# Kernel tuning notes

Measured on AMD Instinct MI355X. Metric: run time of the kernel, lower is better.

Reference implementation:

```python
import jax, jax.numpy as jnp
import numpy as np

D = 128
N_JOB, N_ST, N_MC, N_RB = 100000, 10000, 10000, 5000
E = 500000
RELS = [("cbl", N_ST), ("li", N_ST), ("nd", N_MC), ("eb", N_MC), ("hb", N_RB)]


def setup_inputs() -> dict:
    key = jax.random.key(0)
    ks = iter(jax.random.split(key, 64))
    inp = {
        "x_job": jax.random.normal(next(ks), (N_JOB, D), jnp.float32),
        "x_station": jax.random.normal(next(ks), (N_ST, D), jnp.float32),
        "x_machine": jax.random.normal(next(ks), (N_MC, D), jnp.float32),
        "x_robot": jax.random.normal(next(ks), (N_RB, D), jnp.float32),
    }
    for name, n_dst in RELS:
        inp[f"src_{name}"] = jax.random.randint(next(ks), (E,), 0, N_JOB, jnp.int32)
        inp[f"dst_{name}"] = jax.random.randint(next(ks), (E,), 0, n_dst, jnp.int32)
        # SAGEConv params: lin_l (with bias) on aggregated neighbors, lin_r (no bias) on dst
        inp[f"Wl_{name}"] = jax.random.normal(next(ks), (D, D), jnp.float32) * 0.02
        inp[f"bl_{name}"] = jnp.zeros((D,), jnp.float32)
        inp[f"Wr_{name}"] = jax.random.normal(next(ks), (D, D), jnp.float32) * 0.02
    return inp


def _sage(x_src, x_dst, src, dst, Wl, bl, Wr):
    # mean-aggregate source features over incoming edges, then linear + root linear
    n_dst = x_dst.shape[0]
    msg = x_src[src]                                                  # [E, D] gather
    agg = jax.ops.segment_sum(msg, dst, num_segments=n_dst)          # [n_dst, D]
    cnt = jax.ops.segment_sum(jnp.ones((src.shape[0],), x_src.dtype), dst, num_segments=n_dst)
    mean = agg / jnp.maximum(cnt, 1.0)[:, None]                       # isolated nodes -> 0
    return mean @ Wl.T + bl + x_dst @ Wr.T


def reference(x_job, x_station, x_machine, x_robot,
              src_cbl, dst_cbl, Wl_cbl, bl_cbl, Wr_cbl,
              src_li, dst_li, Wl_li, bl_li, Wr_li,
              src_nd, dst_nd, Wl_nd, bl_nd, Wr_nd,
              src_eb, dst_eb, Wl_eb, bl_eb, Wr_eb,
              src_hb, dst_hb, Wl_hb, bl_hb, Wr_hb):
    # HeteroConv aggr='sum' over relations sharing a destination type, then ReLU
    h_s = jax.nn.relu(_sage(x_job, x_station, src_cbl, dst_cbl, Wl_cbl, bl_cbl, Wr_cbl)
                      + _sage(x_job, x_station, src_li, dst_li, Wl_li, bl_li, Wr_li))
    h_m = jax.nn.relu(_sage(x_job, x_machine, src_nd, dst_nd, Wl_nd, bl_nd, Wr_nd)
                      + _sage(x_job, x_machine, src_eb, dst_eb, Wl_eb, bl_eb, Wr_eb))
    h_r = jax.nn.relu(_sage(x_job, x_robot, src_hb, dst_hb, Wl_hb, bl_hb, Wr_hb))
    return (h_s, h_m, h_r)
```

## Files before the change

kernel.cpp:

```cpp
#include <hip/hip_runtime.h>
#include <hip/hip_fp8.h>

#define D 128
#define NREL 5
#define E_EDGES 500000
#define NB_PER 313
#define NBTOT 1565
#define ST_CHUNK 8192
#define CAP 2048

typedef float f32x2 __attribute__((ext_vector_type(2)));
typedef __attribute__((ext_vector_type(8))) short bf16x8;
typedef __attribute__((ext_vector_type(4))) float f32x4;

struct RelIdx {
    const int* src[NREL];
    const int* dst[NREL];
};
struct MeanPtrs { float* mean[NREL]; };

__device__ __forceinline__ int shift_of(int r) { return (r < 4) ? 5 : 4; }

__device__ __forceinline__ unsigned char f32_to_fp8(float f) {
    __hip_fp8_e4m3 h(f);
    return (unsigned char)h.__x;
}
__device__ __forceinline__ float fp8_to_f32(unsigned int b) {
    __hip_fp8_e4m3 h;
    h.__x = (__hip_fp8_storage_t)b;
    return (float)h;
}
__device__ __forceinline__ unsigned short f2bf(float f) {
    unsigned u = __float_as_uint(f);
    unsigned r = (u + 0x7FFFu + ((u >> 16) & 1u)) >> 16;
    return (unsigned short)r;
}
#if defined(__has_builtin)
#if __has_builtin(__builtin_amdgcn_cvt_pk_f32_fp8)
#define HAVE_PK_CVT 1
#endif
#endif
template<bool HI>
__device__ __forceinline__ f32x2 pk8(unsigned u) {
#ifdef HAVE_PK_CVT
    return __builtin_amdgcn_cvt_pk_f32_fp8(u, HI);
#else
    unsigned s = HI ? (u >> 16) : u;
    f32x2 r; r.x = fp8_to_f32(s & 0xFF); r.y = fp8_to_f32((s >> 8) & 0xFF);
    return r;
#endif
}

struct PrepArgs {
    const float* Wl[NREL]; const float* Wr[NREL]; const float* bl[NREL];
    unsigned short* Bt0; unsigned short* Bt1; unsigned short* Bt2;
    float* bias;
};

struct FusedAArgs {
    RelIdx ri;
    int* bucket_cnt;
    const float* x_job; unsigned char* x_f8; int do_cvt;
    PrepArgs P;
    int nb_hist, nb_cvt;
};

__global__ __launch_bounds__(256) void fusedA_kernel(FusedAArgs A) {
    const int b = blockIdx.x;
    const int tid = threadIdx.x;
    if (b < A.nb_hist) {
        __shared__ int lh[NBTOT];
        for (int i = tid; i < NBTOT; i += 256) lh[i] = 0;
        __syncthreads();
        int e0 = (b * 256 + tid) * 4;
        if (e0 < E_EDGES) {
            #pragma unroll
            for (int r = 0; r < NREL; ++r) {
                int4 d4 = *reinterpret_cast<const int4*>(A.ri.dst[r] + e0);
                int sh = shift_of(r);
                atomicAdd(&lh[NB_PER * r + (d4.x >> sh)], 1);
                atomicAdd(&lh[NB_PER * r + (d4.y >> sh)], 1);
                atomicAdd(&lh[NB_PER * r + (d4.z >> sh)], 1);
                atomicAdd(&lh[NB_PER * r + (d4.w >> sh)], 1);
            }
        }
        __syncthreads();
        for (int i = tid; i < NBTOT; i += 256)
            if (lh[i]) atomicAdd(&A.bucket_cnt[i], lh[i]);
    } else if (b < A.nb_hist + A.nb_cvt) {
        if (!A.do_cvt) return;
        int t = (b - A.nb_hist) * 256 + tid;
        const int n8 = 100000 * D / 8;
        if (t >= n8) return;
        const float4* x4 = reinterpret_cast<const float4*>(A.x_job);
        float4 va = x4[2 * t], vb = x4[2 * t + 1];
        uint2 o;
        o.x = (unsigned)f32_to_fp8(va.x) | ((unsigned)f32_to_fp8(va.y) << 8)
            | ((unsigned)f32_to_fp8(va.z) << 16) | ((unsigned)f32_to_fp8(va.w) << 24);
        o.y = (unsigned)f32_to_fp8(vb.x) | ((unsigned)f32_to_fp8(vb.y) << 8)
            | ((unsigned)f32_to_fp8(vb.z) << 16) | ((unsigned)f32_to_fp8(vb.w) << 24);
        reinterpret_cast<uint2*>(A.x_f8)[t] = o;
    } else {
        int idx = (b - A.nb_hist - A.nb_cvt) * 256 + tid;
        const PrepArgs& P = A.P;
        if (idx < 49152) {
            int j = idx / 384, k = idx - j * 384;
            float v;
            if (k < 128)      v = P.Wl[0][j * D + k];
            else if (k < 256) v = P.Wl[1][j * D + (k - 128)];
            else              v = P.Wr[0][j * D + (k - 256)] + P.Wr[1][j * D + (k - 256)];
            P.Bt0[idx] = f2bf(v);
        } else if (idx < 98304) {
            int l = idx - 49152;
            int j = l / 384, k = l - j * 384;
            float v;
            if (k < 128)      v = P.Wl[2][j * D + k];
            else if (k < 256) v = P.Wl[3][j * D + (k - 128)];
            else              v = P.Wr[2][j * D + (k - 256)] + P.Wr[3][j * D + (k - 256)];
            P.Bt1[l] = f2bf(v);
        } else if (idx < 131072) {
            int l = idx - 98304;
            int j = l >> 8, k = l & 255;
            float v = (k < 128) ? P.Wl[4][j * D + k] : P.Wr[4][j * D + (k - 128)];
            P.Bt2[l] = f2bf(v);
        } else if (idx < 131456) {
            int l = idx - 131072;
            int t2 = l >> 7, j = l & 127;
            float v = (t2 == 0) ? P.bl[0][j] + P.bl[1][j]
                    : (t2 == 1) ? P.bl[2][j] + P.bl[3][j]
                                : P.bl[4][j];
            P.bias[l] = v;
        }
    }
}

__global__ __launch_bounds__(1024) void bucket_scan_kernel(
    const int* __restrict__ bucket_cnt, int* __restrict__ bucket_base,
    int* __restrict__ cur_b)
{
    __shared__ int s[1024];
    const int tid = threadIdx.x;
    const int i0 = 2 * tid, i1 = 2 * tid + 1;
    int c0 = (i0 < NBTOT) ? bucket_cnt[i0] : 0;
    int c1 = (i1 < NBTOT) ? bucket_cnt[i1] : 0;
    s[tid] = c0 + c1;
    __syncthreads();
    for (int d = 1; d < 1024; d <<= 1) {
        int t = (tid >= d) ? s[tid - d] : 0;
        __syncthreads();
        s[tid] += t;
        __syncthreads();
    }
    int exp_ = s[tid] - (c0 + c1);
    if (i0 < NBTOT) { bucket_base[i0] = exp_;      cur_b[i0] = exp_; }
    if (i1 < NBTOT) { bucket_base[i1] = exp_ + c0; cur_b[i1] = exp_ + c0; }
    if (tid == 1023) bucket_base[NBTOT] = s[1023];
}

__global__ __launch_bounds__(512) void stage_block_kernel(
    RelIdx idx, int* __restrict__ cur_b, int* __restrict__ stage)
{
    __shared__ int hist[NB_PER], gbase[NB_PER], lcur[NB_PER];
    const int tid = threadIdx.x;
    const int nchunk = (E_EDGES + ST_CHUNK - 1) / ST_CHUNK;
    const int r = blockIdx.x / nchunk;
    const int c = blockIdx.x - r * nchunk;
    const int e_beg = c * ST_CHUNK;
    const int e_end = min(e_beg + ST_CHUNK, E_EDGES);
    const int sh = shift_of(r);
    const int lmask = (1 << sh) - 1;
    for (int i = tid; i < NB_PER; i += 512) { hist[i] = 0; lcur[i] = 0; }
    __syncthreads();
    const int* dp = idx.dst[r];
    const int* sp = idx.src[r];

    int4 dreg[4];
    #pragma unroll
    for (int it = 0; it < 4; ++it) {
        int e = e_beg + tid * 4 + it * 2048;
        if (e + 4 <= e_end) {
            int4 d4 = *reinterpret_cast<const int4*>(dp + e);
            dreg[it] = d4;
            atomicAdd(&hist[d4.x >> sh], 1);
            atomicAdd(&hist[d4.y >> sh], 1);
            atomicAdd(&hist[d4.z >> sh], 1);
            atomicAdd(&hist[d4.w >> sh], 1);
        } else {
            for (int q = e; q < e_end; ++q) atomicAdd(&hist[dp[q] >> sh], 1);
        }
    }
    __syncthreads();

    for (int i = tid; i < NB_PER; i += 512)
        if (hist[i] > 0) gbase[i] = atomicAdd(&cur_b[NB_PER * r + i], hist[i]);
    __syncthreads();

    #pragma unroll
    for (int it = 0; it < 4; ++it) {
        int e = e_beg + tid * 4 + it * 2048;
        if (e + 4 <= e_end) {
            int4 d4 = dreg[it];
            int4 s4 = *reinterpret_cast<const int4*>(sp + e);
            int b0 = d4.x >> sh, p0 = gbase[b0] + atomicAdd(&lcur[b0], 1);
            stage[p0] = ((d4.x & lmask) << 20) | s4.x;
            int b1 = d4.y >> sh, p1 = gbase[b1] + atomicAdd(&lcur[b1], 1);
            stage[p1] = ((d4.y & lmask) << 20) | s4.y;
            int b2 = d4.z >> sh, p2 = gbase[b2] + atomicAdd(&lcur[b2], 1);
            stage[p2] = ((d4.z & lmask) << 20) | s4.z;
            int b3 = d4.w >> sh, p3 = gbase[b3] + atomicAdd(&lcur[b3], 1);
            stage[p3] = ((d4.w & lmask) << 20) | s4.w;
        } else {
            for (int q = e; q < e_end; ++q) {
                int dq = dp[q];
                int bq = dq >> sh, pq = gbase[bq] + atomicAdd(&lcur[bq], 1);
                stage[pq] = ((dq & lmask) << 20) | sp[q];
            }
        }
    }
}

template<bool FP8>
__global__ __launch_bounds__(256) void gather_bucket_kernel(
    const int* __restrict__ stage, const int* __restrict__ bucket_base,
    const void* __restrict__ xsrc, MeanPtrs mp)
{
    __shared__ int srt[CAP];
    __shared__ int h[32], ex[33], cur[32];
    const int b = blockIdx.x;
    const int tid = threadIdx.x;
    const int r = b / NB_PER;
    const int lb = b - NB_PER * r;
    const int sh = shift_of(r);
    const int ndst_r = (r < 4) ? 10000 : 5000;
    const int dst0 = lb << sh;
    const int nreal = min(1 << sh, ndst_r - dst0);
    const int seg0 = bucket_base[b];
    const int len = bucket_base[b + 1] - seg0;

    if (tid < 32) { h[tid] = 0; cur[tid] = 0; }
    __syncthreads();
    for (int p = tid; p < len; p += 256)
        atomicAdd(&h[stage[seg0 + p] >> 20], 1);
    __syncthreads();
    int c0 = (tid < 32) ? h[tid] : 0;
    for (int d = 1; d < 32; d <<= 1) {
        int t = (tid < 32 && tid >= d) ? h[tid - d] : 0;
        __syncthreads();
        if (tid < 32) h[tid] += t;
        __syncthreads();
    }
    if (tid < 32) ex[tid] = h[tid] - c0;
    if (tid == 0) ex[32] = len;
    __syncthreads();
    if (len <= CAP) {
        for (int p = tid; p < len; p += 256) {
            int v = stage[seg0 + p];
            int dl = v >> 20;
            int k = atomicAdd(&cur[dl], 1);
            srt[ex[dl] + k] = v & 0xFFFFF;
        }
    }
    __syncthreads();

    const int wave = tid >> 6, lane = tid & 63;
    float* mout = mp.mean[r];

    if (FP8) {
        const int quarter = lane >> 4, sub = lane & 15;
        const unsigned char* x8 = (const unsigned char*)xsrc;
        const unsigned char* xbase = x8 + sub * 8;
        for (int dl = wave; dl < nreal; dl += 4) {
            int s = ex[dl], e2 = ex[dl + 1];
            float4 aA = {0.f, 0.f, 0.f, 0.f};
            float4 aB = {0.f, 0.f, 0.f, 0.f};
            if (len <= CAP) {
                int k = s;
                for (; k + 8 <= e2; k += 8) {
                    int i0 = srt[k + quarter];
                    int i1 = srt[k + 4 + quarter];
                    uint2 u0 = *reinterpret_cast<const uint2*>(xbase + (size_t)i0 * D);
                    uint2 u1 = *reinterpret_cast<const uint2*>(xbase + (size_t)i1 * D);
                    f32x2 p0 = pk8<false>(u0.x), p1 = pk8<true>(u0.x);
                    f32x2 p2 = pk8<false>(u0.y), p3 = pk8<true>(u0.y);
                    f32x2 q0 = pk8<false>(u1.x), q1 = pk8<true>(u1.x);
                    f32x2 q2 = pk8<false>(u1.y), q3 = pk8<true>(u1.y);
                    aA.x += p0.x + q0.x; aA.y += p0.y + q0.y;
                    aA.z += p1.x + q1.x; aA.w += p1.y + q1.y;
                    aB.x += p2.x + q2.x; aB.y += p2.y + q2.y;
                    aB.z += p3.x + q3.x; aB.w += p3.y + q3.y;
                }
                for (; k < e2; k += 4) {
                    if (k + quarter < e2) {
                        int i0 = srt[k + quarter];
                        uint2 u = *reinterpret_cast<const uint2*>(xbase + (size_t)i0 * D);
                        f32x2 p0 = pk8<false>(u.x), p1 = pk8<true>(u.x);
                        f32x2 p2 = pk8<false>(u.y), p3 = pk8<true>(u.y);
                        aA.x += p0.x; aA.y += p0.y; aA.z += p1.x; aA.w += p1.y;
                        aB.x += p2.x; aB.y += p2.y; aB.z += p3.x; aB.w += p3.y;
                    }
                }
            } else {
                if (quarter == 0) {
                    for (int p = 0; p < len; ++p) {
                        int v = stage[seg0 + p];
                        if ((v >> 20) == dl) {
                            uint2 u = *reinterpret_cast<const uint2*>(
                                xbase + (size_t)(v & 0xFFFFF) * D);
                            f32x2 p0 = pk8<false>(u.x), p1 = pk8<true>(u.x);
                            f32x2 p2 = pk8<false>(u.y), p3 = pk8<true>(u.y);
                            aA.x += p0.x; aA.y += p0.y; aA.z += p1.x; aA.w += p1.y;
                            aB.x += p2.x; aB.y += p2.y; aB.z += p3.x; aB.w += p3.y;
                        }
                    }
                }
            }
            aA.x += __shfl_xor(aA.x, 16); aA.y += __shfl_xor(aA.y, 16);
            aA.z += __shfl_xor(aA.z, 16); aA.w += __shfl_xor(aA.w, 16);
            aB.x += __shfl_xor(aB.x, 16); aB.y += __shfl_xor(aB.y, 16);
            aB.z += __shfl_xor(aB.z, 16); aB.w += __shfl_xor(aB.w, 16);
            aA.x += __shfl_xor(aA.x, 32); aA.y += __shfl_xor(aA.y, 32);
            aA.z += __shfl_xor(aA.z, 32); aA.w += __shfl_xor(aA.w, 32);
            aB.x += __shfl_xor(aB.x, 32); aB.y += __shfl_xor(aB.y, 32);
            aB.z += __shfl_xor(aB.z, 32); aB.w += __shfl_xor(aB.w, 32);
            if (quarter == 0) {
                float inv = 1.0f / (float)max(e2 - s, 1);
                float4 m0, m1;
                m0.x = aA.x * inv; m0.y = aA.y * inv; m0.z = aA.z * inv; m0.w = aA.w * inv;
                m1.x = aB.x * inv; m1.y = aB.y * inv; m1.z = aB.z * inv; m1.w = aB.w * inv;
                float* orow = mout + (size_t)(dst0 + dl) * D + sub * 8;
                *reinterpret_cast<float4*>(orow) = m0;
                *reinterpret_cast<float4*>(orow + 4) = m1;
            }
        }
    } else {
        const float* basef = (const float*)xsrc + lane * 2;
        for (int dl = wave; dl < nreal; dl += 4) {
            int s = ex[dl], e2 = ex[dl + 1];
            float ax = 0.f, ay = 0.f;
            if (len <= CAP) {
                for (int k = s; k < e2; ++k) {
                    float2 v = *reinterpret_cast<const float2*>(basef + (size_t)srt[k] * D);
                    ax += v.x; ay += v.y;
                }
            } else {
                for (int p = 0; p < len; ++p) {
                    int v = stage[seg0 + p];
                    if ((v >> 20) == dl) {
                        float2 vv = *reinterpret_cast<const float2*>(basef + (size_t)(v & 0xFFFFF) * D);
                        ax += vv.x; ay += vv.y;
                    }
                }
            }
            float inv = 1.0f / (float)max(e2 - s, 1);
            float2 m; m.x = ax * inv; m.y = ay * inv;
            *reinterpret_cast<float2*>(mout + (size_t)(dst0 + dl) * D + lane * 2) = m;
        }
    }
}

struct GemmArgs {
    const float* Asrc[3][3];
    const unsigned short* Bt[3];
    const float* bias[3];
    float* out[3];
    int M[3]; int K[3]; int blk_start[3];
};

__global__ __launch_bounds__(256) void sage_gemm_kernel(GemmArgs A) {
    __shared__ unsigned short sA[64][40];
    __shared__ unsigned short sB[128][40];

    int b = blockIdx.x;
    int ty_ = (b >= A.blk_start[1]) + (b >= A.blk_start[2]);
    int mb = b - A.blk_start[ty_];
    const int M = A.M[ty_];
    const int K = A.K[ty_];
    const int row0 = mb * 64;
    const unsigned short* Bt = A.Bt[ty_];

    const int tid = threadIdx.x;
    const int lane = tid & 63;
    const int wave = tid >> 6;

    f32x4 acc[8];
    #pragma unroll
    for (int t = 0; t < 8; ++t) acc[t] = (f32x4){0.f, 0.f, 0.f, 0.f};

    for (int kc = 0; kc < K; kc += 32) {
        if (kc) __syncthreads();
        const float* src = A.Asrc[ty_][kc >> 7];
        const int c0 = kc & 127;

        {
            int r = tid >> 2, kg = (tid & 3) * 8;
            int grow = row0 + r; if (grow >= M) grow = M - 1;
            const float* p = src + (size_t)grow * D + c0 + kg;
            float4 v0 = *reinterpret_cast<const float4*>(p);
            float4 v1 = *reinterpret_cast<const float4*>(p + 4);
            uint4 w;
            w.x = (unsigned)f2bf(v0.x) | ((unsigned)f2bf(v0.y) << 16);
            w.y = (unsigned)f2bf(v0.z) | ((unsigned)f2bf(v0.w) << 16);
            w.z = (unsigned)f2bf(v1.x) | ((unsigned)f2bf(v1.y) << 16);
            w.w = (unsigned)f2bf(v1.z) | ((unsigned)f2bf(v1.w) << 16);
            *reinterpret_cast<uint4*>(&sA[r][kg]) = w;
        }
        #pragma unroll
        for (int i = 0; i < 2; ++i) {
            int s = tid + i * 256;
            int r = s >> 2, kg = (s & 3) * 8;
            *reinterpret_cast<uint4*>(&sB[r][kg]) =
                *reinterpret_cast<const uint4*>(Bt + (size_t)r * K + kc + kg);
        }
        __syncthreads();

        bf16x8 af = *reinterpret_cast<const bf16x8*>(&sA[wave * 16 + (lane & 15)][(lane >> 4) * 8]);
        #pragma unroll
        for (int t = 0; t < 8; ++t) {
            bf16x8 bfr = *reinterpret_cast<const bf16x8*>(&sB[t * 16 + (lane & 15)][(lane >> 4) * 8]);
            acc[t] = __builtin_amdgcn_mfma_f32_16x16x32_bf16(af, bfr, acc[t], 0, 0, 0);
        }
    }

    const float* bias = A.bias[ty_];
    float* out = A.out[ty_];
    const int c = lane & 15;
    const int rbase = wave * 16 + (lane >> 4) * 4;
    #pragma unroll
    for (int t = 0; t < 8; ++t) {
        int col = t * 16 + c;
        float bv = bias[col];
        #pragma unroll
        for (int q = 0; q < 4; ++q) {
            int grow = row0 + rbase + q;
            if (grow < M)
                out[(size_t)grow * D + col] = fmaxf(acc[t][q] + bv, 0.f);
        }
    }
}

extern "C" void kernel_launch(void* const* d_in, const int* in_sizes, int n_in,
                              void* d_out, int out_size, void* d_ws, size_t ws_size,
                              hipStream_t stream) {
    const float* x_job = (const float*)d_in[0];
    const float* x_st  = (const float*)d_in[1];
    const float* x_mc  = (const float*)d_in[2];
    const float* x_rb  = (const float*)d_in[3];

    const int N_JOB = 100000, N_ST = 10000, N_MC = 10000, N_RB = 5000;
    const int E = E_EDGES;

    RelIdx ri;
    const float* Wl[NREL]; const float* bl[NREL]; const float* Wr[NREL];
    for (int r = 0; r < NREL; ++r) {
        ri.src[r] = (const int*)  d_in[4 + r * 5 + 0];
        ri.dst[r] = (const int*)  d_in[4 + r * 5 + 1];
        Wl[r]     = (const float*)d_in[4 + r * 5 + 2];
        bl[r]     = (const float*)d_in[4 + r * 5 + 3];
        Wr[r]     = (const float*)d_in[4 + r * 5 + 4];
    }

    int* wsi = (int*)d_ws;
    float* wsf = (float*)d_ws;
    size_t off = 0;
    int* bucket_cnt  = wsi + off; off += NBTOT;
    int* bucket_base = wsi + off; off += NBTOT + 1;
    int* cur_b       = wsi + off; off += NBTOT;
    int* stage       = wsi + off; off += (size_t)NREL * E;
    float* mean_st_b = wsf + off; off += (size_t)N_ST * D;
    float* mean_mc_b = wsf + off; off += (size_t)N_MC * D;
    unsigned short* Bt0 = (unsigned short*)(wsi + off); off += 49152 / 2;
    unsigned short* Bt1 = (unsigned short*)(wsi + off); off += 49152 / 2;
    unsigned short* Bt2 = (unsigned short*)(wsi + off); off += 32768 / 2;
    float* bsum = wsf + off; off += 3 * 128;
    unsigned char* x_f8 = (unsigned char*)(wsi + off);
    size_t off_f8_end = off + (size_t)N_JOB * D / 4;
    const bool use_fp8 = (off_f8_end * sizeof(int) <= ws_size);

    float* out = (float*)d_out;
    MeanPtrs mp;
    mp.mean[0] = out;
    mp.mean[1] = mean_st_b;
    mp.mean[2] = out + (size_t)N_ST * D;
    mp.mean[3] = mean_mc_b;
    mp.mean[4] = out + (size_t)(N_ST + N_MC) * D;

    (void)hipMemsetAsync(bucket_cnt, 0, NBTOT * sizeof(int), stream);

    FusedAArgs FA;
    FA.ri = ri;
    FA.bucket_cnt = bucket_cnt;
    FA.x_job = x_job; FA.x_f8 = x_f8; FA.do_cvt = use_fp8 ? 1 : 0;
    for (int r = 0; r < NREL; ++r) { FA.P.Wl[r] = Wl[r]; FA.P.Wr[r] = Wr[r]; FA.P.bl[r] = bl[r]; }
    FA.P.Bt0 = Bt0; FA.P.Bt1 = Bt1; FA.P.Bt2 = Bt2; FA.P.bias = bsum;
    FA.nb_hist = (E / 4 + 255) / 256;
    FA.nb_cvt  = (N_JOB * D / 8 + 255) / 256;
    int nb_prep = (131456 + 255) / 256;
    fusedA_kernel<<<FA.nb_hist + FA.nb_cvt + nb_prep, 256, 0, stream>>>(FA);

    bucket_scan_kernel<<<1, 1024, 0, stream>>>(bucket_cnt, bucket_base, cur_b);

    const int nchunk = (E + ST_CHUNK - 1) / ST_CHUNK;
    stage_block_kernel<<<NREL * nchunk, 512, 0, stream>>>(ri, cur_b, stage);

    if (use_fp8)
        gather_bucket_kernel<true><<<NBTOT, 256, 0, stream>>>(stage, bucket_base, x_f8, mp);
    else
        gather_bucket_kernel<false><<<NBTOT, 256, 0, stream>>>(stage, bucket_base, x_job, mp);

    GemmArgs GA;
    GA.Asrc[0][0] = mp.mean[0]; GA.Asrc[0][1] = mp.mean[1]; GA.Asrc[0][2] = x_st;
    GA.Asrc[1][0] = mp.mean[2]; GA.Asrc[1][1] = mp.mean[3]; GA.Asrc[1][2] = x_mc;
    GA.Asrc[2][0] = mp.mean[4]; GA.Asrc[2][1] = x_rb;       GA.Asrc[2][2] = x_rb;
    GA.Bt[0] = Bt0; GA.Bt[1] = Bt1; GA.Bt[2] = Bt2;
    GA.bias[0] = bsum; GA.bias[1] = bsum + 128; GA.bias[2] = bsum + 256;
    GA.out[0] = out;
    GA.out[1] = out + (size_t)N_ST * D;
    GA.out[2] = out + (size_t)(N_ST + N_MC) * D;
    GA.M[0] = N_ST; GA.M[1] = N_MC; GA.M[2] = N_RB;
    GA.K[0] = 384;  GA.K[1] = 384;  GA.K[2] = 256;
    int nb0 = (N_ST + 63) / 64, nb1 = (N_MC + 63) / 64, nb2 = (N_RB + 63) / 64;
    GA.blk_start[0] = 0;
    GA.blk_start[1] = nb0;
    GA.blk_start[2] = nb0 + nb1;

    sage_gemm_kernel<<<nb0 + nb1 + nb2, 256, 0, stream>>>(GA);
}
```

Measured before the change: 146.2 us.

## Split FP8 job features into four 32-column planes for cache-local gathers

The FP8 copy of x_job is stored as four column planes of 32 bytes per node instead of one 128-byte row per node. The gather-mean loop now takes one plane at a time, with 16 edges per wave and 4 lanes per edge, so each pass touches a 3.2 MB plane that is more likely to stay in L2 or the last-level cache. The cost is that every edge index list is read four times and the shuffle reduction is deeper. Each gather request is also a smaller 32-byte sector, so sector efficiency may drop.

Result: slower. 161.8 us (+10.7%).

```diff
diff --git a/kernel.cpp b/kernel.cpp
--- a/kernel.cpp
+++ b/kernel.cpp
@@ -8,6 +8,7 @@
 #define NBTOT 1565
 #define ST_CHUNK 8192
 #define CAP 2048
+#define N_JOB_C 100000
 
 typedef float f32x2 __attribute__((ext_vector_type(2)));
 typedef __attribute__((ext_vector_type(8))) short bf16x8;
@@ -90,16 +91,20 @@
     } else if (b < A.nb_hist + A.nb_cvt) {
         if (!A.do_cvt) return;
         int t = (b - A.nb_hist) * 256 + tid;
-        const int n8 = 100000 * D / 8;
-        if (t >= n8) return;
-        const float4* x4 = reinterpret_cast<const float4*>(A.x_job);
-        float4 va = x4[2 * t], vb = x4[2 * t + 1];
+        const int nq = N_JOB_C * 4;
+        if (t >= 4 * nq) return;
+        int q = t / nq;
+        int rem = t - q * nq;
+        int n = rem >> 2, sub = rem & 3;
+        const float* p = A.x_job + (size_t)n * D + q * 32 + sub * 8;
+        float4 va = *reinterpret_cast<const float4*>(p);
+        float4 vb = *reinterpret_cast<const float4*>(p + 4);
         uint2 o;
         o.x = (unsigned)f32_to_fp8(va.x) | ((unsigned)f32_to_fp8(va.y) << 8)
             | ((unsigned)f32_to_fp8(va.z) << 16) | ((unsigned)f32_to_fp8(va.w) << 24);
         o.y = (unsigned)f32_to_fp8(vb.x) | ((unsigned)f32_to_fp8(vb.y) << 8)
             | ((unsigned)f32_to_fp8(vb.z) << 16) | ((unsigned)f32_to_fp8(vb.w) << 24);
-        reinterpret_cast<uint2*>(A.x_f8)[t] = o;
+        *reinterpret_cast<uint2*>(A.x_f8 + (size_t)q * N_JOB_C * 32 + (size_t)n * 32 + sub * 8) = o;
     } else {
         int idx = (b - A.nb_hist - A.nb_cvt) * 256 + tid;
         const PrepArgs& P = A.P;
@@ -266,70 +271,72 @@
     float* mout = mp.mean[r];
 
     if (FP8) {
-        const int quarter = lane >> 4, sub = lane & 15;
+        const int eidx = lane >> 2, sub = lane & 3;
         const unsigned char* x8 = (const unsigned char*)xsrc;
-        const unsigned char* xbase = x8 + sub * 8;
-        for (int dl = wave; dl < nreal; dl += 4) {
-            int s = ex[dl], e2 = ex[dl + 1];
-            float4 aA = {0.f, 0.f, 0.f, 0.f};
-            float4 aB = {0.f, 0.f, 0.f, 0.f};
-            if (len <= CAP) {
-                int k = s;
-                for (; k + 8 <= e2; k += 8) {
-                    int i0 = srt[k + quarter];
-                    int i1 = srt[k + 4 + quarter];
-                    uint2 u0 = *reinterpret_cast<const uint2*>(xbase + (size_t)i0 * D);
-                    uint2 u1 = *reinterpret_cast<const uint2*>(xbase + (size_t)i1 * D);
-                    f32x2 p0 = pk8<false>(u0.x), p1 = pk8<true>(u0.x);
-                    f32x2 p2 = pk8<false>(u0.y), p3 = pk8<true>(u0.y);
-                    f32x2 q0 = pk8<false>(u1.x), q1 = pk8<true>(u1.x);
-                    f32x2 q2 = pk8<false>(u1.y), q3 = pk8<true>(u1.y);
-                    aA.x += p0.x + q0.x; aA.y += p0.y + q0.y;
-                    aA.z += p1.x + q1.x; aA.w += p1.y + q1.y;
-                    aB.x += p2.x + q2.x; aB.y += p2.y + q2.y;
-                    aB.z += p3.x + q3.x; aB.w += p3.y + q3.y;
-                }
-                for (; k < e2; k += 4) {
-                    if (k + quarter < e2) {
-                        int i0 = srt[k + quarter];
-                        uint2 u = *reinterpret_cast<const uint2*>(xbase + (size_t)i0 * D);
-                        f32x2 p0 = pk8<false>(u.x), p1 = pk8<true>(u.x);
-                        f32x2 p2 = pk8<false>(u.y), p3 = pk8<true>(u.y);
-                        aA.x += p0.x; aA.y += p0.y; aA.z += p1.x; aA.w += p1.y;
-                        aB.x += p2.x; aB.y += p2.y; aB.z += p3.x; aB.w += p3.y;
+        #pragma unroll
+        for (int qp = 0; qp < 4; ++qp) {
+            const unsigned char* plane = x8 + (size_t)qp * N_JOB_C * 32 + sub * 8;
+            for (int dl = wave; dl < nreal; dl += 4) {
+                int s = ex[dl], e2 = ex[dl + 1];
+                float4 a = {0.f, 0.f, 0.f, 0.f};
+                float4 b2 = {0.f, 0.f, 0.f, 0.f};
+                if (len <= CAP) {
+                    int k = s;
+                    for (; k + 32 <= e2; k += 32) {
+                        int i0 = srt[k + eidx];
+                        int i1 = srt[k + 16 + eidx];
+                        uint2 u0 = *reinterpret_cast<const uint2*>(plane + (size_t)i0 * 32);
+                        uint2 u1 = *reinterpret_cast<const uint2*>(plane + (size_t)i1 * 32);
+                        f32x2 p0 = pk8<false>(u0.x), p1 = pk8<true>(u0.x);
+                        f32x2 p2 = pk8<false>(u0.y), p3 = pk8<true>(u0.y);
+                        f32x2 q0 = pk8<false>(u1.x), q1 = pk8<true>(u1.x);
+                        f32x2 q2 = pk8<false>(u1.y), q3 = pk8<true>(u1.y);
+                        a.x += p0.x + q0.x; a.y += p0.y + q0.y;
+                        a.z += p1.x + q1.x; a.w += p1.y + q1.y;
+                        b2.x += p2.x + q2.x; b2.y += p2.y + q2.y;
+                        b2.z += p3.x + q3.x; b2.w += p3.y + q3.y;
                     }
-                }
-            } else {
-                if (quarter == 0) {
-                    for (int p = 0; p < len; ++p) {
-                        int v = stage[seg0 + p];
-                        if ((v >> 20) == dl) {
-                            uint2 u = *reinterpret_cast<const uint2*>(
-                                xbase + (size_t)(v & 0xFFFFF) * D);
+                    for (; k < e2; k += 16) {
+                        if (k + eidx < e2) {
+                            int i0 = srt[k + eidx];
+                            uint2 u = *reinterpret_cast<const uint2*>(plane + (size_t)i0 * 32);
                             f32x2 p0 = pk8<false>(u.x), p1 = pk8<true>(u.x);
                             f32x2 p2 = pk8<false>(u.y), p3 = pk8<true>(u.y);
-                            aA.x += p0.x; aA.y += p0.y; aA.z += p1.x; aA.w += p1.y;
-                            aB.x += p2.x; aB.y += p2.y; aB.z += p3.x; aB.w += p3.y;
+                            a.x += p0.x; a.y += p0.y; a.z += p1.x; a.w += p1.y;
+                            b2.x += p2.x; b2.y += p2.y; b2.z += p3.x; b2.w += p3.y;
+                        }
+                    }
+                } else {
+                    if (eidx == 0) {
+                        for (int p = 0; p < len; ++p) {
+                            int v = stage[seg0 + p];
+                            if ((v >> 20) == dl) {
+                                uint2 u = *reinterpret_cast<const uint2*>(
+                                    plane + (size_t)(v & 0xFFFFF) * 32);
+                                f32x2 p0 = pk8<false>(u.x), p1 = pk8<true>(u.x);
+                                f32x2 p2 = pk8<false>(u.y), p3 = pk8<true>(u.y);
+                                a.x += p0.x; a.y += p0.y; a.z += p1.x; a.w += p1.y;
+                                b2.x += p2.x; b2.y += p2.y; b2.z += p3.x; b2.w += p3.y;
+                            }
                         }
                     }
                 }
-            }
-            aA.x += __shfl_xor(aA.x, 16); aA.y += __shfl_xor(aA.y, 16);
-            aA.z += __shfl_xor(aA.z, 16); aA.w += __shfl_xor(aA.w, 16);
-            aB.x += __shfl_xor(aB.x, 16); aB.y += __shfl_xor(aB.y, 16);
-            aB.z += __shfl_xor(aB.z, 16); aB.w += __shfl_xor(aB.w, 16);
-            aA.x += __shfl_xor(aA.x, 32); aA.y += __shfl_xor(aA.y, 32);
-            aA.z += __shfl_xor(aA.z, 32); aA.w += __shfl_xor(aA.w, 32);
-            aB.x += __shfl_xor(aB.x, 32); aB.y += __shfl_xor(aB.y, 32);
-            aB.z += __shfl_xor(aB.z, 32); aB.w += __shfl_xor(aB.w, 32);
-            if (quarter == 0) {
-                float inv = 1.0f / (float)max(e2 - s, 1);
-                float4 m0, m1;
-                m0.x = aA.x * inv; m0.y = aA.y * inv; m0.z = aA.z * inv; m0.w = aA.w * inv;
-                m1.x = aB.x * inv; m1.y = aB.y * inv; m1.z = aB.z * inv; m1.w = aB.w * inv;
-                float* orow = mout + (size_t)(dst0 + dl) * D + sub * 8;
-                *reinterpret_cast<float4*>(orow) = m0;
-                *reinterpret_cast<float4*>(orow + 4) = m1;
+                #pragma unroll
+                for (int d2 = 4; d2 <= 32; d2 <<= 1) {
+                    a.x += __shfl_xor(a.x, d2);  a.y += __shfl_xor(a.y, d2);
+                    a.z += __shfl_xor(a.z, d2);  a.w += __shfl_xor(a.w, d2);
+                    b2.x += __shfl_xor(b2.x, d2); b2.y += __shfl_xor(b2.y, d2);
+                    b2.z += __shfl_xor(b2.z, d2); b2.w += __shfl_xor(b2.w, d2);
+                }
+                if (eidx == 0) {
+                    float inv = 1.0f / (float)max(e2 - s, 1);
+                    float4 m0, m1;
+                    m0.x = a.x * inv;  m0.y = a.y * inv;  m0.z = a.z * inv;  m0.w = a.w * inv;
+                    m1.x = b2.x * inv; m1.y = b2.y * inv; m1.z = b2.z * inv; m1.w = b2.w * inv;
+                    float* orow = mout + (size_t)(dst0 + dl) * D + qp * 32 + sub * 8;
+                    *reinterpret_cast<float4*>(orow) = m0;
+                    *reinterpret_cast<float4*>(orow + 4) = m1;
+                }
             }
         }
     } else {
@@ -446,7 +453,7 @@
     const float* x_mc  = (const float*)d_in[2];
     const float* x_rb  = (const float*)d_in[3];
 
-    const int N_JOB = 100000, N_ST = 10000, N_MC = 10000, N_RB = 5000;
+    const int N_JOB = N_JOB_C, N_ST = 10000, N_MC = 10000, N_RB = 5000;
     const int E = E_EDGES;
 
     RelIdx ri;
```
